# Performance work log

Hardware: AMD Instinct MI355X
Metric: run time of the kernel (lower is better)

Reference implementation:

```python
import jax, jax.numpy as jnp
import numpy as np

N = 100000
R = 32
E = 3200000
EMB = 128
H = 32
B = 16
C = 16

def setup_inputs() -> dict:
    key = jax.random.key(0)
    ks = jax.random.split(key, 10)
    def xavier(k, shape):
        fan_in, fan_out = shape[-2], shape[-1]
        gain = jnp.sqrt(2.0)  # relu gain
        std = gain * jnp.sqrt(2.0 / (fan_in + fan_out))
        return jax.random.normal(k, shape, jnp.float32) * std
    return {
        'embeddings': xavier(ks[0], (N, EMB)),
        'comps1': xavier(ks[1], (R, B)),
        'bases1': xavier(ks[2], (B, EMB, H)),
        'comps2': xavier(ks[3], (R, B)),
        'bases2': xavier(ks[4], (B, H, C)),
        'bias1': jnp.zeros((H,), jnp.float32),
        'bias2': jnp.zeros((C,), jnp.float32),
        'rel': jax.random.randint(ks[5], (E,), 0, R, jnp.int32),
        'fr': jax.random.randint(ks[6], (E,), 0, N, jnp.int32),
        'to': jax.random.randint(ks[7], (E,), 0, N, jnp.int32),
    }

def reference(embeddings, comps1, bases1, comps2, bases2, bias1, bias2, rel, fr, to):
    n, emb = embeddings.shape
    r = comps1.shape[0]
    h = bases1.shape[2]
    # edge normalization: vals = 1 / rowsum of vertical adjacency, row = rel*n + fr
    seg = rel * n + fr  # [E]
    deg = jax.ops.segment_sum(jnp.ones_like(fr, jnp.float32), seg, num_segments=r * n)
    vals = 1.0 / deg[seg]  # [E]
    # layer 1: basis-composed weights, per-relation transform, hor-graph spmm
    w1 = jnp.einsum('rb,beh->reh', comps1, bases1)          # [r,emb,h]
    xw = jnp.einsum('ne,reh->rnh', embeddings, w1)           # [r,n,h]
    # hor_graph @ xw.view(r*n,h): hidden1[fr] += vals * xw[rel, to]
    hidden1 = jax.ops.segment_sum(vals[:, None] * xw[rel, to], fr, num_segments=n)  # [n,h]
    hidden1 = jax.nn.relu(hidden1 + bias1)
    # layer 2: ver-graph spmm then relation-combining einsum
    w2 = jnp.einsum('rb,bhc->rhc', comps2, bases2)           # [r,h,c]
    hidden2 = jax.ops.segment_sum(vals[:, None] * hidden1[to], seg, num_segments=r * n)
    hidden2 = hidden2.reshape(r, n, h)
    out = jnp.einsum('rhc,rnh->nc', w2, hidden2)             # [n,c]
    return out + bias2
```

## Files before the change

### kernel.cpp

```cpp
#include <hip/hip_runtime.h>

#define N_NODES 100000
#define N_PAD   100096
#define E_EDGES 3200000
#define NB      392
#define BCAP    12288
#define EPB     8192

typedef float f32x4 __attribute__((ext_vector_type(4)));
typedef __bf16 bf16x8 __attribute__((ext_vector_type(8)));

__device__ __forceinline__ float b2f(unsigned int u) {
    union { unsigned int i; float f; } x; x.i = u << 16; return x.f;
}
__device__ __forceinline__ unsigned short f2b(float f) {
    union { float f; unsigned int i; } x; x.f = f;
    unsigned int u = x.i + 0x7FFFu + ((x.i >> 16) & 1u);
    return (unsigned short)(u >> 16);
}

__global__ __launch_bounds__(256) void kcur(int* __restrict__ gCursor) {
    int id = blockIdx.x * 256 + threadIdx.x;
    if (id < NB) gCursor[id] = id * BCAP;
}

__global__ __launch_bounds__(256) void kemb(const float* __restrict__ emb,
                                            unsigned short* __restrict__ embb) {
    int id = blockIdx.x * 256 + threadIdx.x;
    if (id >= N_PAD * 128 / 8) return;
    size_t base = (size_t)id * 8;
    ushort4 o0 = {0, 0, 0, 0}, o1 = {0, 0, 0, 0};
    if (base < (size_t)N_NODES * 128) {
        float4 v0 = *(const float4*)(emb + base);
        float4 v1 = *(const float4*)(emb + base + 4);
        o0.x = f2b(v0.x); o0.y = f2b(v0.y); o0.z = f2b(v0.z); o0.w = f2b(v0.w);
        o1.x = f2b(v1.x); o1.y = f2b(v1.y); o1.z = f2b(v1.z); o1.w = f2b(v1.w);
    }
    *(ushort4*)(embb + base) = o0;
    *(ushort4*)(embb + base + 4) = o1;
}

__global__ __launch_bounds__(256) void kw1(const float* __restrict__ comps1,
                                           const float* __restrict__ bases1,
                                           unsigned short* __restrict__ w1T) {
    int id = blockIdx.x * 256 + threadIdx.x;
    if (id >= 1024 * 128) return;
    int k = id & 127, j = id >> 7;
    int r = j >> 5, h = j & 31;
    float s = 0.f;
#pragma unroll
    for (int b = 0; b < 16; b++)
        s += comps1[r * 16 + b] * bases1[b * 4096 + k * 32 + h];
    w1T[(size_t)j * 128 + k] = f2b(s);
}

__global__ __launch_bounds__(256) void kw2(const float* __restrict__ comps2,
                                           const float* __restrict__ bases2,
                                           unsigned short* __restrict__ w2T) {
    int id = blockIdx.x * 256 + threadIdx.x;
    if (id >= 512 * 32) return;
    int h = id & 31, j = id >> 5;
    int r = j >> 4, c = j & 15;
    float s = 0.f;
#pragma unroll
    for (int b = 0; b < 16; b++)
        s += comps2[r * 16 + b] * bases2[b * 512 + h * 16 + c];
    w2T[(size_t)j * 32 + h] = f2b(s);
}

__global__ __launch_bounds__(256) void kbinA(const int* __restrict__ rel,
                                             const int* __restrict__ fr,
                                             const int* __restrict__ to,
                                             int* __restrict__ gCursor,
                                             unsigned int* __restrict__ stage) {
    __shared__ int cnt[NB];
    __shared__ int lexcl[NB + 1];
    __shared__ int sdelta[NB];
    __shared__ int sa[512], sb_[512];
    __shared__ unsigned int sortbuf[EPB];
    int tid = threadIdx.x;
    int g40 = blockIdx.x * (EPB / 4);
    unsigned int w_[32];
    int bk[32];
    for (int i = tid; i < NB; i += 256) cnt[i] = 0;
    __syncthreads();
#pragma unroll
    for (int i = 0; i < 8; i++) {
        int g4 = g40 + i * 256 + tid;
        if (g4 < E_EDGES / 4) {
            int4 f4 = ((const int4*)fr)[g4];
            int4 r4 = ((const int4*)rel)[g4];
            int4 t4 = ((const int4*)to)[g4];
            int fa[4] = {f4.x, f4.y, f4.z, f4.w};
            int ra[4] = {r4.x, r4.y, r4.z, r4.w};
            int ta[4] = {t4.x, t4.y, t4.z, t4.w};
#pragma unroll
            for (int u = 0; u < 4; u++) {
                int b = fa[u] >> 8;
                w_[i * 4 + u] = ((unsigned int)(fa[u] & 255) << 22) |
                                ((unsigned int)ra[u] << 17) | (unsigned int)ta[u];
                bk[i * 4 + u] = b;
                atomicAdd(&cnt[b], 1);
            }
        } else {
#pragma unroll
            for (int u = 0; u < 4; u++) bk[i * 4 + u] = -1;
        }
    }
    __syncthreads();
    sa[tid] = (tid < NB) ? cnt[tid] : 0;
    sa[tid + 256] = (tid + 256 < NB) ? cnt[tid + 256] : 0;
    __syncthreads();
    int* src = sa; int* dst = sb_;
    for (int ofs = 1; ofs < 512; ofs <<= 1) {
        int x0 = src[tid];
        if (tid >= ofs) x0 += src[tid - ofs];
        int x1 = src[tid + 256] + src[tid + 256 - ofs];
        __syncthreads();
        dst[tid] = x0; dst[tid + 256] = x1;
        __syncthreads();
        int* tmp = src; src = dst; dst = tmp;
    }
    for (int b = tid; b < NB; b += 256) {
        int c = cnt[b];
        int lex = src[b] - c;
        lexcl[b] = lex;
        int gb = 0;
        if (c) gb = atomicAdd(&gCursor[b], c);
        sdelta[b] = gb - lex;
        cnt[b] = 0;
    }
    if (tid == 0) lexcl[NB] = src[NB - 1];
    __syncthreads();
#pragma unroll
    for (int i = 0; i < 32; i++) {
        if (bk[i] >= 0) {
            int rank = atomicAdd(&cnt[bk[i]], 1);
            sortbuf[lexcl[bk[i]] + rank] = w_[i];
        }
    }
    __syncthreads();
    int wv = tid >> 6, lane = tid & 63;
    for (int b = wv; b < NB; b += 4) {
        int s = lexcl[b], e = lexcl[b + 1];
        int d = sdelta[b];
        for (int i = s + lane; i < e; i += 64)
            stage[d + i] = sortbuf[i];
    }
}

__global__ __launch_bounds__(512) void kscan(const int* __restrict__ gCursor,
                                             int* __restrict__ bucketBase) {
    __shared__ int a[512], b[512];
    int t = threadIdx.x;
    int v = (t < NB) ? (gCursor[t] - t * BCAP) : 0;
    a[t] = v;
    __syncthreads();
    int* src = a; int* dst = b;
    for (int ofs = 1; ofs < 512; ofs <<= 1) {
        int x = src[t];
        if (t >= ofs) x += src[t - ofs];
        __syncthreads();
        dst[t] = x;
        __syncthreads();
        int* tmp = src; src = dst; dst = tmp;
    }
    if (t < NB) bucketBase[t] = src[t] - v;
}

__global__ __launch_bounds__(256) void kscatter2(const unsigned int* __restrict__ stage,
                                                 const int* __restrict__ gCursor,
                                                 const int* __restrict__ bucketBase,
                                                 int* __restrict__ rowptr,
                                                 unsigned int* __restrict__ packed) {
    __shared__ int hist[256], hexcl[256], rk[256], sa[256], sb[256];
    __shared__ int hist2[256 * 32];
    int b = blockIdx.x, t = threadIdx.x;
    int nb = gCursor[b] - b * BCAP;
    int sbase = b * BCAP;
    int gbase = bucketBase[b];
    int nb4 = nb >> 2;
    hist[t] = 0; rk[t] = 0;
    for (int i = t; i < 256 * 32; i += 256) hist2[i] = 0;
    __syncthreads();
    for (int i4 = t; i4 < nb4; i4 += 256) {
        uint4 p4 = ((const uint4*)(stage + sbase))[i4];
        unsigned int pa[4] = {p4.x, p4.y, p4.z, p4.w};
#pragma unroll
        for (int u = 0; u < 4; u++) {
            atomicAdd(&hist[pa[u] >> 22], 1);
            atomicAdd(&hist2[((pa[u] >> 22) << 5) | ((pa[u] >> 17) & 31)], 1);
        }
    }
    for (int i = (nb4 << 2) + t; i < nb; i += 256) {
        unsigned int pk = stage[sbase + i];
        atomicAdd(&hist[pk >> 22], 1);
        atomicAdd(&hist2[((pk >> 22) << 5) | ((pk >> 17) & 31)], 1);
    }
    __syncthreads();
    int v = hist[t];
    sa[t] = v;
    __syncthreads();
    int* src = sa; int* dst = sb;
    for (int ofs = 1; ofs < 256; ofs <<= 1) {
        int x = src[t];
        if (t >= ofs) x += src[t - ofs];
        __syncthreads();
        dst[t] = x;
        __syncthreads();
        int* tmp = src; src = dst; dst = tmp;
    }
    int excl = src[t] - v;
    hexcl[t] = excl;
    rowptr[b * 256 + t] = gbase + excl;
    __syncthreads();
    for (int i4 = t; i4 < nb4; i4 += 256) {
        uint4 p4 = ((const uint4*)(stage + sbase))[i4];
        unsigned int pa[4] = {p4.x, p4.y, p4.z, p4.w};
#pragma unroll
        for (int u = 0; u < 4; u++) {
            int frlo = pa[u] >> 22;
            int rank = atomicAdd(&rk[frlo], 1);
            int dg = min(hist2[(frlo << 5) | ((pa[u] >> 17) & 31)], 1023);
            packed[gbase + hexcl[frlo] + rank] = ((unsigned int)dg << 22) | (pa[u] & 0x3FFFFFu);
        }
    }
    for (int i = (nb4 << 2) + t; i < nb; i += 256) {
        unsigned int pk = stage[sbase + i];
        int frlo = pk >> 22;
        int rank = atomicAdd(&rk[frlo], 1);
        int dg = min(hist2[(frlo << 5) | ((pk >> 17) & 31)], 1023);
        packed[gbase + hexcl[frlo] + rank] = ((unsigned int)dg << 22) | (pk & 0x3FFFFFu);
    }
}

__global__ __launch_bounds__(256) void gemm1(const unsigned short* __restrict__ embb,
                                             const unsigned short* __restrict__ w1T,
                                             unsigned short* __restrict__ xw) {
    __shared__ unsigned short ldsT[4 * 16 * 136];
    int id = blockIdx.x;
    int xcd = id & 7, w = id >> 3;
    int bn = w & 15, mgl = w >> 4;
    int mg = mgl * 8 + xcd;
    if (mg >= 98) return;
    int lane = threadIdx.x & 63, wave = threadIdx.x >> 6;
    int m_ = lane & 15, q = lane >> 4;
    unsigned short* tw = &ldsT[wave * 16 * 136];
    bf16x8 B[4][4];
    const unsigned short* Bbase = w1T + (size_t)(bn * 64 + m_) * 128 + q * 8;
#pragma unroll
    for (int j = 0; j < 4; j++)
#pragma unroll
        for (int k0 = 0; k0 < 4; k0++)
            B[j][k0] = *(const bf16x8*)(Bbase + j * 16 * 128 + k0 * 32);
    int mrow0 = mg * 1024 + wave * 16;
    const unsigned short* Abase = embb + (size_t)(mrow0 + m_) * 128 + q * 8;
    bf16x8 a0[4], a1[4];
    if (mrow0 < N_PAD) {
#pragma unroll
        for (int k0 = 0; k0 < 4; k0++)
            a0[k0] = *(const bf16x8*)(Abase + k0 * 32);
    }
#pragma unroll
    for (int t = 0; t < 16; t++) {
        int m0 = mrow0 + t * 64;
        if (m0 >= N_PAD) break;
        bf16x8* acur = (t & 1) ? a1 : a0;
        bf16x8* anext = (t & 1) ? a0 : a1;
        if (t < 15 && m0 + 64 < N_PAD) {
#pragma unroll
            for (int k0 = 0; k0 < 4; k0++)
                anext[k0] = *(const bf16x8*)(Abase + (size_t)(t + 1) * 64 * 128 + k0 * 32);
        }
        f32x4 acc[4] = {};
#pragma unroll
        for (int k0 = 0; k0 < 4; k0++)
#pragma unroll
            for (int j = 0; j < 4; j++)
                acc[j] = __builtin_amdgcn_mfma_f32_16x16x32_bf16(B[j][k0], acur[k0], acc[j], 0, 0, 0);
#pragma unroll
        for (int jj = 0; jj < 4; jj++) {
            ushort4 s;
            s.x = f2b(acc[jj][0]); s.y = f2b(acc[jj][1]);
            s.z = f2b(acc[jj][2]); s.w = f2b(acc[jj][3]);
            *(ushort4*)(tw + m_ * 136 + jj * 16 + q * 4) = s;
        }
        __asm__ volatile("s_waitcnt lgkmcnt(0)" ::: "memory");
#pragma unroll
        for (int ri = 0; ri < 2; ri++) {
            int row = (lane >> 3) + ri * 8;
            int c = lane & 7;
            uint4 v = *(const uint4*)(tw + row * 136 + c * 8);
            int grow = m0 + row;
            if (grow < N_NODES)
                *(uint4*)(xw + (size_t)grow * 1024 + bn * 64 + c * 8) = v;
        }
        __asm__ volatile("s_waitcnt lgkmcnt(0)" ::: "memory");
    }
}

__global__ __launch_bounds__(256) void edge1csr(const unsigned int* __restrict__ packed,
                                                const int* __restrict__ rowptr,
                                                const unsigned short* __restrict__ xw,
                                                const float* __restrict__ bias1,
                                                unsigned short* __restrict__ h1b) {
    __shared__ unsigned int ebuf[4 * 64];
    __shared__ float vbuf[4 * 64];
    int wave = threadIdx.x >> 6, lane = threadIdx.x & 63;
    int f = blockIdx.x * 4 + wave;
    if (f >= N_NODES) return;
    int s = rowptr[f], k = rowptr[f + 1] - s;
    int sub = lane & 7, p = lane >> 3;
    f32x4 acc = {0.f, 0.f, 0.f, 0.f};
    for (int base = 0; base < k; base += 64) {
        int e = base + lane;
        if (e < k) {
            unsigned int pk = packed[s + e];
            ebuf[wave * 64 + lane] = pk;
            vbuf[wave * 64 + lane] = 1.0f / (float)(pk >> 22);
        }
        int cnum = min(64, k - base);
        int nst = (cnum + 7) >> 3;
#pragma unroll 4
        for (int i = 0; i < nst; i++) {
            int ei = (i << 3) + p;
            if (ei < cnum) {
                unsigned int pk = ebuf[wave * 64 + ei];
                float v = vbuf[wave * 64 + ei];
                int t_ = pk & 0x1FFFF, r = (pk >> 17) & 31;
                ushort4 raw = *(const ushort4*)(xw + (size_t)t_ * 1024 + (r << 5) + (sub << 2));
                acc.x += v * b2f(raw.x); acc.y += v * b2f(raw.y);
                acc.z += v * b2f(raw.z); acc.w += v * b2f(raw.w);
            }
        }
    }
#pragma unroll
    for (int ofs = 8; ofs < 64; ofs <<= 1) {
        acc.x += __shfl_xor(acc.x, ofs, 64);
        acc.y += __shfl_xor(acc.y, ofs, 64);
        acc.z += __shfl_xor(acc.z, ofs, 64);
        acc.w += __shfl_xor(acc.w, ofs, 64);
    }
    if (p == 0) {
        int h = sub << 2;
        ushort4 o;
        o.x = f2b(fmaxf(acc.x + bias1[h + 0], 0.f));
        o.y = f2b(fmaxf(acc.y + bias1[h + 1], 0.f));
        o.z = f2b(fmaxf(acc.z + bias1[h + 2], 0.f));
        o.w = f2b(fmaxf(acc.w + bias1[h + 3], 0.f));
        *(ushort4*)(h1b + (size_t)f * 32 + h) = o;
    }
}

__global__ __launch_bounds__(256) void gemm2(const unsigned short* __restrict__ h1b,
                                             const unsigned short* __restrict__ w2T,
                                             unsigned short* __restrict__ z) {
    __shared__ unsigned short ldsT[4 * 16 * 136];
    int id = blockIdx.x;
    int xcd = id & 7, w = id >> 3;
    int bn = w & 7, mgl = w >> 3;
    int mg = mgl * 8 + xcd;
    if (mg >= 98) return;
    int lane = threadIdx.x & 63, wave = threadIdx.x >> 6;
    int m_ = lane & 15, q = lane >> 4;
    unsigned short* tw = &ldsT[wave * 16 * 136];
    bf16x8 B[4];
    const unsigned short* Bbase = w2T + (size_t)(bn * 64 + m_) * 32 + q * 8;
#pragma unroll
    for (int j = 0; j < 4; j++)
        B[j] = *(const bf16x8*)(Bbase + j * 16 * 32);
    int mrow0 = mg * 1024 + wave * 32;
    const unsigned short* Abase = h1b + (size_t)(mrow0 + m_) * 32 + q * 8;
    bf16x8 a0[2], a1[2];
    if (mrow0 < N_PAD) {
        a0[0] = *(const bf16x8*)(Abase);
        a0[1] = *(const bf16x8*)(Abase + 16 * 32);
    }
#pragma unroll
    for (int t = 0; t < 8; t++) {
        int m0 = mrow0 + t * 128;
        if (m0 >= N_PAD) break;
        bf16x8* acur = (t & 1) ? a1 : a0;
        bf16x8* anext = (t & 1) ? a0 : a1;
        if (t < 7 && m0 + 128 < N_PAD) {
            anext[0] = *(const bf16x8*)(Abase + (size_t)(t + 1) * 128 * 32);
            anext[1] = *(const bf16x8*)(Abase + (size_t)(t + 1) * 128 * 32 + 16 * 32);
        }
        f32x4 acc[2][4] = {};
#pragma unroll
        for (int i = 0; i < 2; i++)
#pragma unroll
            for (int j = 0; j < 4; j++)
                acc[i][j] = __builtin_amdgcn_mfma_f32_16x16x32_bf16(B[j], acur[i], acc[i][j], 0, 0, 0);
#pragma unroll
        for (int i = 0; i < 2; i++) {
#pragma unroll
            for (int jj = 0; jj < 4; jj++) {
                ushort4 s;
                s.x = f2b(acc[i][jj][0]); s.y = f2b(acc[i][jj][1]);
                s.z = f2b(acc[i][jj][2]); s.w = f2b(acc[i][jj][3]);
                *(ushort4*)(tw + m_ * 136 + jj * 16 + q * 4) = s;
            }
            __asm__ volatile("s_waitcnt lgkmcnt(0)" ::: "memory");
#pragma unroll
            for (int ri = 0; ri < 2; ri++) {
                int row = (lane >> 3) + ri * 8;
                int c = lane & 7;
                uint4 v = *(const uint4*)(tw + row * 136 + c * 8);
                int grow = m0 + i * 16 + row;
                if (grow < N_NODES)
                    *(uint4*)(z + (size_t)grow * 512 + bn * 64 + c * 8) = v;
            }
            __asm__ volatile("s_waitcnt lgkmcnt(0)" ::: "memory");
        }
    }
}

__global__ __launch_bounds__(256) void edge2csr(const unsigned int* __restrict__ packed,
                                                const int* __restrict__ rowptr,
                                                const unsigned short* __restrict__ z,
                                                const float* __restrict__ bias2,
                                                float* __restrict__ out) {
    __shared__ unsigned int ebuf[4 * 64];
    __shared__ float vbuf[4 * 64];
    int wave = threadIdx.x >> 6, lane = threadIdx.x & 63;
    int f = blockIdx.x * 4 + wave;
    if (f >= N_NODES) return;
    int s = rowptr[f], k = rowptr[f + 1] - s;
    int sub = lane & 3, p = lane >> 2;
    f32x4 acc = {0.f, 0.f, 0.f, 0.f};
    for (int base = 0; base < k; base += 64) {
        int e = base + lane;
        if (e < k) {
            unsigned int pk = packed[s + e];
            ebuf[wave * 64 + lane] = pk;
            vbuf[wave * 64 + lane] = 1.0f / (float)(pk >> 22);
        }
        int cnum = min(64, k - base);
        int nst = (cnum + 15) >> 4;
#pragma unroll 4
        for (int i = 0; i < nst; i++) {
            int ei = (i << 4) + p;
            if (ei < cnum) {
                unsigned int pk = ebuf[wave * 64 + ei];
                float v = vbuf[wave * 64 + ei];
                int t_ = pk & 0x1FFFF, r = (pk >> 17) & 31;
                ushort4 raw = *(const ushort4*)(z + (size_t)t_ * 512 + (r << 4) + (sub << 2));
                acc.x += v * b2f(raw.x); acc.y += v * b2f(raw.y);
                acc.z += v * b2f(raw.z); acc.w += v * b2f(raw.w);
            }
        }
    }
#pragma unroll
    for (int ofs = 4; ofs < 64; ofs <<= 1) {
        acc.x += __shfl_xor(acc.x, ofs, 64);
        acc.y += __shfl_xor(acc.y, ofs, 64);
        acc.z += __shfl_xor(acc.z, ofs, 64);
        acc.w += __shfl_xor(acc.w, ofs, 64);
    }
    if (p == 0) {
        int c = sub << 2;
        float4 o;
        o.x = acc.x + bias2[c + 0];
        o.y = acc.y + bias2[c + 1];
        o.z = acc.z + bias2[c + 2];
        o.w = acc.w + bias2[c + 3];
        *(float4*)(out + (size_t)f * 16 + c) = o;
    }
}

extern "C" void kernel_launch(void* const* d_in, const int* in_sizes, int n_in,
                              void* d_out, int out_size, void* d_ws, size_t ws_size,
                              hipStream_t stream) {
    (void)in_sizes; (void)n_in; (void)out_size; (void)ws_size;
    const float* emb    = (const float*)d_in[0];
    const float* comps1 = (const float*)d_in[1];
    const float* bases1 = (const float*)d_in[2];
    const float* comps2 = (const float*)d_in[3];
    const float* bases2 = (const float*)d_in[4];
    const float* bias1  = (const float*)d_in[5];
    const float* bias2  = (const float*)d_in[6];
    const int* rel = (const int*)d_in[7];
    const int* fr  = (const int*)d_in[8];
    const int* to  = (const int*)d_in[9];
    float* out = (float*)d_out;
    char* ws = (char*)d_ws;

    int* gCursor         = (int*)(ws);
    int* bucketBase      = (int*)(ws + 2048);
    int* rowptr          = (int*)(ws + 4096);
    unsigned int* packed = (unsigned int*)(ws + 406528);
    unsigned short* h1b  = (unsigned short*)(ws + 13206528);
    unsigned short* w1T  = (unsigned short*)(ws + 19612672);
    unsigned short* w2T  = (unsigned short*)(ws + 19874816);
    unsigned short* embb = (unsigned short*)(ws + 19907584);
    unsigned short* xw   = (unsigned short*)(ws + 45532160);
    unsigned short* z    = xw;
    unsigned int* stage  = (unsigned int*)xw;

    kcur<<<2, 256, 0, stream>>>(gCursor);
    kemb<<<6256, 256, 0, stream>>>(emb, embb);
    kw1<<<512, 256, 0, stream>>>(comps1, bases1, w1T);
    kw2<<<64, 256, 0, stream>>>(comps2, bases2, w2T);
    kbinA<<<(E_EDGES + EPB - 1) / EPB, 256, 0, stream>>>(rel, fr, to, gCursor, stage);
    kscan<<<1, 512, 0, stream>>>(gCursor, bucketBase);
    kscatter2<<<NB, 256, 0, stream>>>(stage, gCursor, bucketBase, rowptr, packed);
    gemm1<<<1664, 256, 0, stream>>>(embb, w1T, xw);
    edge1csr<<<25000, 256, 0, stream>>>(packed, rowptr, xw, bias1, h1b);
    gemm2<<<832, 256, 0, stream>>>(h1b, w2T, z);
    edge2csr<<<25000, 256, 0, stream>>>(packed, rowptr, z, bias2, out);
}
```

Baseline: 425.5 us.

## Restructure gemm1 tiles so waves share rows and write 512-byte row segments

gemm1 now assigns the four waves of a block to four adjacent 64-column output slices of the same 16-row tile. Before, each wave handled a different row range for one slice. The waves stage results in a shared LDS tile so each output row gets a contiguous 512-byte store instead of 128-byte pieces, which should coalesce the large xw write better. Float-to-bf16 conversion uses the packed v_cvt_pk_bf16_f32 instruction instead of manual rounding. The cost is two __syncthreads per iteration, and the XCD-aware block swizzle is dropped.

```diff
diff --git a/kernel.cpp b/kernel.cpp
--- a/kernel.cpp
+++ b/kernel.cpp
@@ -17,6 +17,11 @@
     union { float f; unsigned int i; } x; x.f = f;
     unsigned int u = x.i + 0x7FFFu + ((x.i >> 16) & 1u);
     return (unsigned short)(u >> 16);
+}
+__device__ __forceinline__ unsigned int cvt2(float lo, float hi) {
+    unsigned int r;
+    asm("v_cvt_pk_bf16_f32 %0, %1, %2" : "=v"(r) : "v"(lo), "v"(hi));
+    return r;
 }
 
 __global__ __launch_bounds__(256) void kcur(int* __restrict__ gCursor) {
@@ -237,15 +242,14 @@
 __global__ __launch_bounds__(256) void gemm1(const unsigned short* __restrict__ embb,
                                              const unsigned short* __restrict__ w1T,
                                              unsigned short* __restrict__ xw) {
-    __shared__ unsigned short ldsT[4 * 16 * 136];
+    __shared__ unsigned short tile[16 * 260];
     int id = blockIdx.x;
-    int xcd = id & 7, w = id >> 3;
-    int bn = w & 15, mgl = w >> 4;
-    int mg = mgl * 8 + xcd;
-    if (mg >= 98) return;
+    int bn4 = id & 3, mg = id >> 2;
+    int mrow0 = mg * 256;
+    if (mrow0 >= N_PAD) return;
     int lane = threadIdx.x & 63, wave = threadIdx.x >> 6;
+    int bn = bn4 * 4 + wave;
     int m_ = lane & 15, q = lane >> 4;
-    unsigned short* tw = &ldsT[wave * 16 * 136];
     bf16x8 B[4][4];
     const unsigned short* Bbase = w1T + (size_t)(bn * 64 + m_) * 128 + q * 8;
 #pragma unroll
@@ -253,24 +257,20 @@
 #pragma unroll
         for (int k0 = 0; k0 < 4; k0++)
             B[j][k0] = *(const bf16x8*)(Bbase + j * 16 * 128 + k0 * 32);
-    int mrow0 = mg * 1024 + wave * 16;
     const unsigned short* Abase = embb + (size_t)(mrow0 + m_) * 128 + q * 8;
     bf16x8 a0[4], a1[4];
-    if (mrow0 < N_PAD) {
-#pragma unroll
-        for (int k0 = 0; k0 < 4; k0++)
-            a0[k0] = *(const bf16x8*)(Abase + k0 * 32);
-    }
+#pragma unroll
+    for (int k0 = 0; k0 < 4; k0++)
+        a0[k0] = *(const bf16x8*)(Abase + k0 * 32);
 #pragma unroll
     for (int t = 0; t < 16; t++) {
-        int m0 = mrow0 + t * 64;
-        if (m0 >= N_PAD) break;
+        int m0 = mrow0 + t * 16;
         bf16x8* acur = (t & 1) ? a1 : a0;
         bf16x8* anext = (t & 1) ? a0 : a1;
-        if (t < 15 && m0 + 64 < N_PAD) {
+        if (t < 15) {
 #pragma unroll
             for (int k0 = 0; k0 < 4; k0++)
-                anext[k0] = *(const bf16x8*)(Abase + (size_t)(t + 1) * 64 * 128 + k0 * 32);
+                anext[k0] = *(const bf16x8*)(Abase + (size_t)(t + 1) * 16 * 128 + k0 * 32);
         }
         f32x4 acc[4] = {};
 #pragma unroll
@@ -280,22 +280,22 @@
                 acc[j] = __builtin_amdgcn_mfma_f32_16x16x32_bf16(B[j][k0], acur[k0], acc[j], 0, 0, 0);
 #pragma unroll
         for (int jj = 0; jj < 4; jj++) {
-            ushort4 s;
-            s.x = f2b(acc[jj][0]); s.y = f2b(acc[jj][1]);
-            s.z = f2b(acc[jj][2]); s.w = f2b(acc[jj][3]);
-            *(ushort4*)(tw + m_ * 136 + jj * 16 + q * 4) = s;
-        }
-        __asm__ volatile("s_waitcnt lgkmcnt(0)" ::: "memory");
-#pragma unroll
-        for (int ri = 0; ri < 2; ri++) {
-            int row = (lane >> 3) + ri * 8;
-            int c = lane & 7;
-            uint4 v = *(const uint4*)(tw + row * 136 + c * 8);
+            uint2 s;
+            s.x = cvt2(acc[jj][0], acc[jj][1]);
+            s.y = cvt2(acc[jj][2], acc[jj][3]);
+            *(uint2*)(tile + m_ * 260 + wave * 64 + jj * 16 + q * 4) = s;
+        }
+        __syncthreads();
+#pragma unroll
+        for (int half = 0; half < 2; half++) {
+            int idx = threadIdx.x + half * 256;
+            int row = idx >> 5, c16 = idx & 31;
+            uint4 v = *(const uint4*)(tile + row * 260 + c16 * 8);
             int grow = m0 + row;
             if (grow < N_NODES)
-                *(uint4*)(xw + (size_t)grow * 1024 + bn * 64 + c * 8) = v;
-        }
-        __asm__ volatile("s_waitcnt lgkmcnt(0)" ::: "memory");
+                *(uint4*)(xw + (size_t)grow * 1024 + bn4 * 256 + c16 * 8) = v;
+        }
+        __syncthreads();
     }
 }
 
@@ -505,7 +505,7 @@
     kbinA<<<(E_EDGES + EPB - 1) / EPB, 256, 0, stream>>>(rel, fr, to, gCursor, stage);
     kscan<<<1, 512, 0, stream>>>(gCursor, bucketBase);
     kscatter2<<<NB, 256, 0, stream>>>(stage, gCursor, bucketBase, rowptr, packed);
-    gemm1<<<1664, 256, 0, stream>>>(embb, w1T, xw);
+    gemm1<<<1568, 256, 0, stream>>>(embb, w1T, xw);
     edge1csr<<<25000, 256, 0, stream>>>(packed, rowptr, xw, bias1, h1b);
     gemm2<<<832, 256, 0, stream>>>(h1b, w2T, z);
     edge2csr<<<25000, 256, 0, stream>>>(packed, rowptr, z, bias2, out);
```

Measured after the change: 423.8 us. Within noise of the previous version (-0.4%).
